# Kernel optimization log

Hardware: AMD Instinct MI355X
Metric: run time of the kernel (lower is better)

The kernel has to match this reference:

```python
import jax, jax.numpy as jnp
import numpy as np

T_STEPS, BATCH, DH, L = 256, 128, 512, 3  # L=3 is the only shape-consistent conv length (kernel=3, no pad)


def _conv3(x, W, b):
    # Conv1d(Dh->2, k=3) on a length-3 signal == full contraction over (Dh, 3)
    # x: (B, Dh, 3), W: (2, Dh, 3), b: (2,) -> (B, 2, 1)
    out = jnp.einsum('bdl,odl->bo', x, W) + b
    return out[:, :, None]


def setup_inputs() -> dict:
    key = jax.random.key(0)
    ks = jax.random.split(key, 5)
    inputs = jax.random.normal(ks[0], (T_STEPS, BATCH, DH, L), dtype=jnp.float32)
    h0 = jnp.zeros((BATCH, DH, L), jnp.float32)
    c0 = jnp.zeros((BATCH, DH, L), jnp.float32)
    scale = 1.0 / np.sqrt(DH * L).astype(np.float32)
    Wr = jax.random.normal(ks[1], (2, DH, L), jnp.float32) * scale  # recurrent_kernel (orthogonal-ish init)
    br = jnp.full((2,), 0.5, jnp.float32)                           # recurrent bias init 0.5
    Wc = jax.random.normal(ks[2], (2, DH, L), jnp.float32) * scale  # cell_memory_kernel
    bc = jnp.zeros((2,), jnp.float32)                               # cell_memory bias init 0
    Wi = jax.random.normal(ks[3], (2, DH, L), jnp.float32) * scale  # input_kernel
    bi = jax.random.normal(ks[4], (2,), jnp.float32) * scale
    return dict(inputs=inputs, h0=h0, c0=c0, Wr=Wr, br=br, Wc=Wc, bc=bc, Wi=Wi, bi=bi)


def reference(inputs, h0, c0, Wr, br, Wc, bc, Wi, bi):
    sig = jax.nn.sigmoid  # fun_gate

    def step(state, xt):
        h, c = state  # (B, Dh, 3) each
        cm = _conv3(c, Wc, bc)
        Cc, Ch = cm[:, 0:1], cm[:, 1:2]   # (B,1,1) each (chunk(2, dim=1))
        rm = _conv3(h, Wr, br)
        Hc, Hh = rm[:, 0:1], rm[:, 1:2]
        im = _conv3(xt, Wi, bi)
        Xc, Xh = im[:, 0:1], im[:, 1:2]
        gh = (1.0 - sig(Ch)) * Xh + (1.0 - sig(Hh)) * h   # broadcast (B,1,1)*(B,Dh,3)
        gc = (1.0 - sig(Hc)) * Xc + (1.0 - sig(Cc)) * c
        ht = jnp.tanh(gh)  # fun_main
        ct = jnp.tanh(gc)
        return (ht, ct), ht

    (hT, cT), outs = jax.lax.scan(step, (h0, c0), inputs)
    return outs, hT, cT
```

## Files before the change

kernel.cpp:

```cpp
#include <hip/hip_runtime.h>

#define T_STEPS 256
#define BATCH   128
#define FEAT    1536
#define NPAIRS  (T_STEPS * BATCH)

template <int CTRL, int RMASK>
__device__ __forceinline__ float dpp_add_step(float v) {
    int m = __builtin_amdgcn_update_dpp(0, __float_as_int(v), CTRL, RMASK, 0xF, true);
    return v + __int_as_float(m);
}

__device__ __forceinline__ float wave_reduce63(float v) {
    v = dpp_add_step<0x111, 0xF>(v);
    v = dpp_add_step<0x112, 0xF>(v);
    v = dpp_add_step<0x114, 0xF>(v);
    v = dpp_add_step<0x118, 0xF>(v);
    v = dpp_add_step<0x142, 0xA>(v);
    v = dpp_add_step<0x143, 0xC>(v);
    return v;
}

__device__ __forceinline__ float one_minus_sig(float x) {
    float e = __builtin_amdgcn_exp2f(x * 1.4426950408889634f);
    return __builtin_amdgcn_rcpf(1.0f + e);
}

__device__ __forceinline__ float tanh_fast(float x) {
    float e = __builtin_amdgcn_exp2f(x * 2.8853900817779268f);
    return fmaf(-2.0f, __builtin_amdgcn_rcpf(1.0f + e), 1.0f);
}

__device__ __forceinline__ void barrier_lds_only() {
    asm volatile("s_waitcnt lgkmcnt(0)\n\ts_barrier" ::: "memory");
}

__global__ __launch_bounds__(256) void xdot_kernel(
    const float* __restrict__ x,
    const float* __restrict__ Wi,
    const float* __restrict__ bi,
    float* __restrict__ X)
{
    const int p    = blockIdx.x;
    const int tid  = threadIdx.x;
    const int wid  = tid >> 6;
    const int lane = tid & 63;

    __shared__ float red[8];

    const float* xp = x + (size_t)p * FEAT;
    const float4 v4 = ((const float4*)xp)[tid];
    const float2 v2 = ((const float2*)(xp + 1024))[tid];

    const float4 w04 = ((const float4*)Wi)[tid];
    const float2 w02 = ((const float2*)(Wi + 1024))[tid];
    const float4 w14 = ((const float4*)(Wi + FEAT))[tid];
    const float2 w12 = ((const float2*)(Wi + FEAT + 1024))[tid];

    float a0 = v4.x * w04.x + v4.y * w04.y + v4.z * w04.z + v4.w * w04.w
             + v2.x * w02.x + v2.y * w02.y;
    float a1 = v4.x * w14.x + v4.y * w14.y + v4.z * w14.z + v4.w * w14.w
             + v2.x * w12.x + v2.y * w12.y;

    a0 = wave_reduce63(a0);
    a1 = wave_reduce63(a1);
    if (lane == 63) {
        red[wid * 2]     = a0;
        red[wid * 2 + 1] = a1;
    }
    __syncthreads();
    if (tid == 0) {
        const float s0 = red[0] + red[2] + red[4] + red[6] + bi[0];
        const float s1 = red[1] + red[3] + red[5] + red[7] + bi[1];
        const int b = p & (BATCH - 1);
        const int t = p >> 7;
        ((float2*)X)[b * T_STEPS + t] = make_float2(s0, s1);
    }
}

__global__ __launch_bounds__(256) void scan_kernel(
    const float* __restrict__ h0,
    const float* __restrict__ c0,
    const float* __restrict__ Wr, const float* __restrict__ br,
    const float* __restrict__ Wc, const float* __restrict__ bc,
    const float* __restrict__ X,
    float* __restrict__ outs,
    float* __restrict__ hT,
    float* __restrict__ cT)
{
    const int b    = blockIdx.x;
    const int tid  = threadIdx.x;
    const int wid  = tid >> 6;
    const int lane = tid & 63;

    __shared__ float4 red[2][4];
    __shared__ float2 Xsh[T_STEPS];

    Xsh[tid] = ((const float2*)X)[b * T_STEPS + tid];

    const float4 wr0_4 = ((const float4*)Wr)[tid];
    const float4 wr1_4 = ((const float4*)(Wr + FEAT))[tid];
    const float2 wr0_2 = ((const float2*)(Wr + 1024))[tid];
    const float2 wr1_2 = ((const float2*)(Wr + FEAT + 1024))[tid];
    const float4 wc0_4 = ((const float4*)Wc)[tid];
    const float4 wc1_4 = ((const float4*)(Wc + FEAT))[tid];
    const float2 wc0_2 = ((const float2*)(Wc + 1024))[tid];
    const float2 wc1_2 = ((const float2*)(Wc + FEAT + 1024))[tid];
    const float br0 = br[0], br1 = br[1];
    const float bc0 = bc[0], bc1 = bc[1];

    const float* h0b = h0 + (size_t)b * FEAT;
    const float* c0b = c0 + (size_t)b * FEAT;
    float4 h4 = ((const float4*)h0b)[tid];
    float2 h2 = ((const float2*)(h0b + 1024))[tid];
    float4 c4 = ((const float4*)c0b)[tid];
    float2 c2 = ((const float2*)(c0b + 1024))[tid];

    float* op = outs + (size_t)b * FEAT;
    const size_t OSTRIDE = (size_t)BATCH * FEAT;

    __syncthreads();

    auto step = [&](float4* buf, int t) {
        const float2 Xv = Xsh[t];

        float pHc = h4.x * wr0_4.x + h4.y * wr0_4.y + h4.z * wr0_4.z + h4.w * wr0_4.w
                  + h2.x * wr0_2.x + h2.y * wr0_2.y;
        float pHh = h4.x * wr1_4.x + h4.y * wr1_4.y + h4.z * wr1_4.z + h4.w * wr1_4.w
                  + h2.x * wr1_2.x + h2.y * wr1_2.y;
        float pCc = c4.x * wc0_4.x + c4.y * wc0_4.y + c4.z * wc0_4.z + c4.w * wc0_4.w
                  + c2.x * wc0_2.x + c2.y * wc0_2.y;
        float pCh = c4.x * wc1_4.x + c4.y * wc1_4.y + c4.z * wc1_4.z + c4.w * wc1_4.w
                  + c2.x * wc1_2.x + c2.y * wc1_2.y;

        pHc = wave_reduce63(pHc);
        pHh = wave_reduce63(pHh);
        pCc = wave_reduce63(pCc);
        pCh = wave_reduce63(pCh);

        if (lane == 63) {
            buf[wid] = make_float4(pHc, pHh, pCc, pCh);
        }
        barrier_lds_only();
        const float4 r0 = buf[0];
        const float4 r1 = buf[1];
        const float4 r2 = buf[2];
        const float4 r3 = buf[3];
        const float Hc = r0.x + r1.x + r2.x + r3.x + br0;
        const float Hh = r0.y + r1.y + r2.y + r3.y + br1;
        const float Cc = r0.z + r1.z + r2.z + r3.z + bc0;
        const float Ch = r0.w + r1.w + r2.w + r3.w + bc1;

        const float Ah = one_minus_sig(Ch) * Xv.y;
        const float Sh = one_minus_sig(Hh);
        const float Ac = one_minus_sig(Hc) * Xv.x;
        const float Sc = one_minus_sig(Cc);

        h4.x = tanh_fast(fmaf(Sh, h4.x, Ah));
        h4.y = tanh_fast(fmaf(Sh, h4.y, Ah));
        h4.z = tanh_fast(fmaf(Sh, h4.z, Ah));
        h4.w = tanh_fast(fmaf(Sh, h4.w, Ah));
        h2.x = tanh_fast(fmaf(Sh, h2.x, Ah));
        h2.y = tanh_fast(fmaf(Sh, h2.y, Ah));

        c4.x = tanh_fast(fmaf(Sc, c4.x, Ac));
        c4.y = tanh_fast(fmaf(Sc, c4.y, Ac));
        c4.z = tanh_fast(fmaf(Sc, c4.z, Ac));
        c4.w = tanh_fast(fmaf(Sc, c4.w, Ac));
        c2.x = tanh_fast(fmaf(Sc, c2.x, Ac));
        c2.y = tanh_fast(fmaf(Sc, c2.y, Ac));

        ((float4*)op)[tid]          = h4;
        ((float2*)(op + 1024))[tid] = h2;
        op += OSTRIDE;
    };

#pragma unroll 1
    for (int t = 0; t < T_STEPS; t += 2) {
        step(red[0], t);
        step(red[1], t + 1);
    }

    float* hp = hT + (size_t)b * FEAT;
    ((float4*)hp)[tid]          = h4;
    ((float2*)(hp + 1024))[tid] = h2;
    float* cp = cT + (size_t)b * FEAT;
    ((float4*)cp)[tid]          = c4;
    ((float2*)(cp + 1024))[tid] = c2;
}

extern "C" void kernel_launch(void* const* d_in, const int* in_sizes, int n_in,
                              void* d_out, int out_size, void* d_ws, size_t ws_size,
                              hipStream_t stream) {
    const float* inputs = (const float*)d_in[0];
    const float* h0     = (const float*)d_in[1];
    const float* c0     = (const float*)d_in[2];
    const float* Wr     = (const float*)d_in[3];
    const float* br     = (const float*)d_in[4];
    const float* Wc     = (const float*)d_in[5];
    const float* bc     = (const float*)d_in[6];
    const float* Wi     = (const float*)d_in[7];
    const float* bi     = (const float*)d_in[8];

    float* out = (float*)d_out;
    float* X   = (float*)d_ws;

    float* outs = out;
    float* hT   = out + (size_t)NPAIRS * FEAT;
    float* cT   = hT + (size_t)BATCH * FEAT;

    xdot_kernel<<<NPAIRS, 256, 0, stream>>>(inputs, Wi, bi, X);
    scan_kernel<<<BATCH, 256, 0, stream>>>(h0, c0, Wr, br, Wc, bc, X,
                                           outs, hT, cT);
}
```

Baseline: 449.1 us.

## Widen scan kernel to 512 threads with lane-parallel gate evaluation

The recurrent scan now runs 512 threads per batch row, each owning 3 features instead of 6. This shortens the per-step dot products and tanh updates on the serial critical path. The cross-wave reduction grows to 8 partials per gate, so four lanes each compute one sigmoid gate and broadcast it with readlane instead of every thread evaluating all four. Output stores become nontemporal to reduce cache pollution from streaming writes. The cost is more waves taking part in each per-step barrier and longer LDS reduction reads.

Result: no change. 454.2 us (+1.1%).

```diff
diff --git a/kernel.cpp b/kernel.cpp
--- a/kernel.cpp
+++ b/kernel.cpp
@@ -4,6 +4,9 @@
 #define BATCH   128
 #define FEAT    1536
 #define NPAIRS  (T_STEPS * BATCH)
+#define SCAN_THREADS 512
+
+typedef float vf2 __attribute__((ext_vector_type(2)));
 
 template <int CTRL, int RMASK>
 __device__ __forceinline__ float dpp_add_step(float v) {
@@ -33,6 +36,10 @@
 
 __device__ __forceinline__ void barrier_lds_only() {
     asm volatile("s_waitcnt lgkmcnt(0)\n\ts_barrier" ::: "memory");
+}
+
+__device__ __forceinline__ float readlane_f(float v, int lane) {
+    return __int_as_float(__builtin_amdgcn_readlane(__float_as_int(v), lane));
 }
 
 __global__ __launch_bounds__(256) void xdot_kernel(
@@ -78,7 +85,7 @@
     }
 }
 
-__global__ __launch_bounds__(256) void scan_kernel(
+__global__ __launch_bounds__(SCAN_THREADS) void scan_kernel(
     const float* __restrict__ h0,
     const float* __restrict__ c0,
     const float* __restrict__ Wr, const float* __restrict__ br,
@@ -92,46 +99,44 @@
     const int tid  = threadIdx.x;
     const int wid  = tid >> 6;
     const int lane = tid & 63;
-
-    __shared__ float4 red[2][4];
+    const int col  = lane & 3;
+
+    __shared__ float  red[2][32];
     __shared__ float2 Xsh[T_STEPS];
 
-    Xsh[tid] = ((const float2*)X)[b * T_STEPS + tid];
-
-    const float4 wr0_4 = ((const float4*)Wr)[tid];
-    const float4 wr1_4 = ((const float4*)(Wr + FEAT))[tid];
-    const float2 wr0_2 = ((const float2*)(Wr + 1024))[tid];
-    const float2 wr1_2 = ((const float2*)(Wr + FEAT + 1024))[tid];
-    const float4 wc0_4 = ((const float4*)Wc)[tid];
-    const float4 wc1_4 = ((const float4*)(Wc + FEAT))[tid];
-    const float2 wc0_2 = ((const float2*)(Wc + 1024))[tid];
-    const float2 wc1_2 = ((const float2*)(Wc + FEAT + 1024))[tid];
-    const float br0 = br[0], br1 = br[1];
-    const float bc0 = bc[0], bc1 = bc[1];
+    if (tid < T_STEPS) Xsh[tid] = ((const float2*)X)[b * T_STEPS + tid];
+
+    const float2 wr0_2 = ((const float2*)Wr)[tid];
+    const float  wr0_1 = Wr[1024 + tid];
+    const float2 wr1_2 = ((const float2*)(Wr + FEAT))[tid];
+    const float  wr1_1 = (Wr + FEAT)[1024 + tid];
+    const float2 wc0_2 = ((const float2*)Wc)[tid];
+    const float  wc0_1 = Wc[1024 + tid];
+    const float2 wc1_2 = ((const float2*)(Wc + FEAT))[tid];
+    const float  wc1_1 = (Wc + FEAT)[1024 + tid];
+
+    const float bias_c = (col == 0) ? br[0] : (col == 1) ? br[1]
+                       : (col == 2) ? bc[0] : bc[1];
 
     const float* h0b = h0 + (size_t)b * FEAT;
     const float* c0b = c0 + (size_t)b * FEAT;
-    float4 h4 = ((const float4*)h0b)[tid];
-    float2 h2 = ((const float2*)(h0b + 1024))[tid];
-    float4 c4 = ((const float4*)c0b)[tid];
-    float2 c2 = ((const float2*)(c0b + 1024))[tid];
+    float2 h2 = ((const float2*)h0b)[tid];
+    float  h1 = h0b[1024 + tid];
+    float2 c2 = ((const float2*)c0b)[tid];
+    float  c1 = c0b[1024 + tid];
 
     float* op = outs + (size_t)b * FEAT;
     const size_t OSTRIDE = (size_t)BATCH * FEAT;
 
     __syncthreads();
 
-    auto step = [&](float4* buf, int t) {
+    auto step = [&](float* buf, int t) {
         const float2 Xv = Xsh[t];
 
-        float pHc = h4.x * wr0_4.x + h4.y * wr0_4.y + h4.z * wr0_4.z + h4.w * wr0_4.w
-                  + h2.x * wr0_2.x + h2.y * wr0_2.y;
-        float pHh = h4.x * wr1_4.x + h4.y * wr1_4.y + h4.z * wr1_4.z + h4.w * wr1_4.w
-                  + h2.x * wr1_2.x + h2.y * wr1_2.y;
-        float pCc = c4.x * wc0_4.x + c4.y * wc0_4.y + c4.z * wc0_4.z + c4.w * wc0_4.w
-                  + c2.x * wc0_2.x + c2.y * wc0_2.y;
-        float pCh = c4.x * wc1_4.x + c4.y * wc1_4.y + c4.z * wc1_4.z + c4.w * wc1_4.w
-                  + c2.x * wc1_2.x + c2.y * wc1_2.y;
+        float pHc = h2.x * wr0_2.x + h2.y * wr0_2.y + h1 * wr0_1;
+        float pHh = h2.x * wr1_2.x + h2.y * wr1_2.y + h1 * wr1_1;
+        float pCc = c2.x * wc0_2.x + c2.y * wc0_2.y + c1 * wc0_1;
+        float pCh = c2.x * wc1_2.x + c2.y * wc1_2.y + c1 * wc1_1;
 
         pHc = wave_reduce63(pHc);
         pHh = wave_reduce63(pHh);
@@ -139,39 +144,32 @@
         pCh = wave_reduce63(pCh);
 
         if (lane == 63) {
-            buf[wid] = make_float4(pHc, pHh, pCc, pCh);
+            *(float4*)&buf[wid * 4] = make_float4(pHc, pHh, pCc, pCh);
         }
         barrier_lds_only();
-        const float4 r0 = buf[0];
-        const float4 r1 = buf[1];
-        const float4 r2 = buf[2];
-        const float4 r3 = buf[3];
-        const float Hc = r0.x + r1.x + r2.x + r3.x + br0;
-        const float Hh = r0.y + r1.y + r2.y + r3.y + br1;
-        const float Cc = r0.z + r1.z + r2.z + r3.z + bc0;
-        const float Ch = r0.w + r1.w + r2.w + r3.w + bc1;
-
-        const float Ah = one_minus_sig(Ch) * Xv.y;
-        const float Sh = one_minus_sig(Hh);
-        const float Ac = one_minus_sig(Hc) * Xv.x;
-        const float Sc = one_minus_sig(Cc);
-
-        h4.x = tanh_fast(fmaf(Sh, h4.x, Ah));
-        h4.y = tanh_fast(fmaf(Sh, h4.y, Ah));
-        h4.z = tanh_fast(fmaf(Sh, h4.z, Ah));
-        h4.w = tanh_fast(fmaf(Sh, h4.w, Ah));
+
+        float s = bias_c;
+#pragma unroll
+        for (int w = 0; w < 8; ++w) s += buf[w * 4 + col];
+        float g = one_minus_sig(s);
+        const float m = (col == 0) ? Xv.x : (col == 3) ? Xv.y : 1.0f;
+        g *= m;
+
+        const float Ac = readlane_f(g, 0);
+        const float Sh = readlane_f(g, 1);
+        const float Sc = readlane_f(g, 2);
+        const float Ah = readlane_f(g, 3);
+
         h2.x = tanh_fast(fmaf(Sh, h2.x, Ah));
         h2.y = tanh_fast(fmaf(Sh, h2.y, Ah));
-
-        c4.x = tanh_fast(fmaf(Sc, c4.x, Ac));
-        c4.y = tanh_fast(fmaf(Sc, c4.y, Ac));
-        c4.z = tanh_fast(fmaf(Sc, c4.z, Ac));
-        c4.w = tanh_fast(fmaf(Sc, c4.w, Ac));
+        h1   = tanh_fast(fmaf(Sh, h1,   Ah));
         c2.x = tanh_fast(fmaf(Sc, c2.x, Ac));
         c2.y = tanh_fast(fmaf(Sc, c2.y, Ac));
-
-        ((float4*)op)[tid]          = h4;
-        ((float2*)(op + 1024))[tid] = h2;
+        c1   = tanh_fast(fmaf(Sc, c1,   Ac));
+
+        vf2 hv; hv.x = h2.x; hv.y = h2.y;
+        __builtin_nontemporal_store(hv, (vf2*)op + tid);
+        __builtin_nontemporal_store(h1, op + 1024 + tid);
         op += OSTRIDE;
     };
 
@@ -182,11 +180,11 @@
     }
 
     float* hp = hT + (size_t)b * FEAT;
-    ((float4*)hp)[tid]          = h4;
-    ((float2*)(hp + 1024))[tid] = h2;
+    ((float2*)hp)[tid] = h2;
+    hp[1024 + tid]     = h1;
     float* cp = cT + (size_t)b * FEAT;
-    ((float4*)cp)[tid]          = c4;
-    ((float2*)(cp + 1024))[tid] = c2;
+    ((float2*)cp)[tid] = c2;
+    cp[1024 + tid]     = c1;
 }
 
 extern "C" void kernel_launch(void* const* d_in, const int* in_sizes, int n_in,
@@ -210,6 +208,6 @@
     float* cT   = hT + (size_t)BATCH * FEAT;
 
     xdot_kernel<<<NPAIRS, 256, 0, stream>>>(inputs, Wi, bi, X);
-    scan_kernel<<<BATCH, 256, 0, stream>>>(h0, c0, Wr, br, Wc, bc, X,
-                                           outs, hT, cT);
-}
+    scan_kernel<<<BATCH, SCAN_THREADS, 0, stream>>>(h0, c0, Wr, br, Wc, bc, X,
+                                                    outs, hT, cT);
+}
```
